# Kernel tuning notes

Hardware: AMD Instinct MI355X
Metric: run time of the kernel (lower is better)

Reference implementation:

```python
import jax, jax.numpy as jnp
import numpy as np

B, CIN, COUT, IMG = 32, 64, 64, 128


def setup_inputs() -> dict:
    key = jax.random.key(0)
    k1, k2 = jax.random.split(key, 2)
    x = jax.random.normal(k1, (B, CIN, IMG, IMG), dtype=jnp.float32)
    kernel = jax.random.uniform(k2, (COUT, 3, 3), dtype=jnp.float32)
    bias = jnp.zeros((COUT, 1, 1, 1), dtype=jnp.float32)
    return {"x": x, "kernel": kernel, "bias": bias}


def reference(x, kernel, bias):
    # GCLayer math: weight[c, ci, p, q] = kernel[c, di+1, dj+1] for q = neighbor(p)
    # within the 3x3 band (adjacency mask), zero elsewhere; shared across ci.
    # out[b,c,p] = sum_ci sum_q weight[c,ci,p,q] x[b,ci,q] + in_channels*bias[c]
    # == 3x3 cross-correlation (zero pad) of (sum over in-channels of x).
    cin = x.shape[1]
    xs = x.sum(axis=1, keepdims=True)              # [B,1,H,W]
    k = kernel[:, None, :, :]                      # [Cout,1,3,3]
    out = jax.lax.conv_general_dilated(
        xs, k, window_strides=(1, 1), padding=((1, 1), (1, 1)),
        dimension_numbers=("NCHW", "OIHW", "NCHW"))  # [B,Cout,H,W]
    # bias (out,1,1,1) was added before the in-channel sum -> scaled by cin
    out = out + cin * bias.reshape(1, -1, 1, 1)
    return out
```

## Files before the change

### kernel.cpp

```cpp
#include <hip/hip_runtime.h>

#define B_    32
#define CIN_  64
#define COUT_ 64
#define IMG_  128
#define W4_   32
#define PIX4_ 4096
#define NPOS_ (B_ * PIX4_)

__global__ __launch_bounds__(256) void ch_sum2(const float* __restrict__ x,
                                               float* __restrict__ part) {
    const int g   = blockIdx.y;
    const int tid = threadIdx.x;
    const int i0  = blockIdx.x * 512 + tid;
    const int i1  = i0 + 256;
    const int b   = i0 >> 12;
    const int p0  = i0 & (PIX4_ - 1);

    const float4* xp = reinterpret_cast<const float4*>(x)
                     + ((size_t)b * CIN_ + (size_t)g * 32) * PIX4_ + p0;

    float4 a0 = make_float4(0.f, 0.f, 0.f, 0.f);
    float4 a1 = make_float4(0.f, 0.f, 0.f, 0.f);
#pragma unroll 8
    for (int c = 0; c < 32; ++c) {
        float4 v0 = xp[(size_t)c * PIX4_];
        float4 v1 = xp[(size_t)c * PIX4_ + 256];
        a0.x += v0.x; a0.y += v0.y; a0.z += v0.z; a0.w += v0.w;
        a1.x += v1.x; a1.y += v1.y; a1.z += v1.z; a1.w += v1.w;
    }
    float4* pp = reinterpret_cast<float4*>(part) + (size_t)g * NPOS_;
    pp[i0] = a0;
    pp[i1] = a1;
}

__global__ __launch_bounds__(256) void conv_shfl(const float* __restrict__ part,
                                                 const float* __restrict__ kern,
                                                 const float* __restrict__ bias,
                                                 float* __restrict__ out) {
    const int n   = blockIdx.x;
    const int swz = (n & 7) * 512 + (n >> 3);
    const int co   = swz & 63;
    const int half = (swz >> 6) & 1;
    const int b    = swz >> 7;
    const int tid  = threadIdx.x;
    const int w4   = tid & 31;
    const int rb   = (tid >> 5) * 8;
    const int r0   = half * 64;

    const float4* p0 = reinterpret_cast<const float4*>(part) + (size_t)b * PIX4_;
    const float4* p1 = p0 + (size_t)NPOS_;

    float4 C[10];
#pragma unroll
    for (int r = 0; r < 10; ++r) {
        const int row = r0 + rb - 1 + r;
        float4 v = make_float4(0.f, 0.f, 0.f, 0.f);
        if (row >= 0 && row < IMG_) {
            float4 u0 = p0[row * W4_ + w4];
            float4 u1 = p1[row * W4_ + w4];
            v = make_float4(u0.x + u1.x, u0.y + u1.y, u0.z + u1.z, u0.w + u1.w);
        }
        C[r] = v;
    }

    float Lw[10], Rx[10];
#pragma unroll
    for (int r = 0; r < 10; ++r) {
        float lw = __shfl_up(C[r].w, 1, 32);
        float rx = __shfl_down(C[r].x, 1, 32);
        Lw[r] = (w4 > 0)  ? lw : 0.f;
        Rx[r] = (w4 < 31) ? rx : 0.f;
    }

    const float* kw = kern + co * 9;
    const float k0 = kw[0], k1 = kw[1], k2 = kw[2];
    const float k3 = kw[3], k4 = kw[4], k5 = kw[5];
    const float k6 = kw[6], k7 = kw[7], k8 = kw[8];
    const float bv = (float)CIN_ * bias[co];

    float4* outp = reinterpret_cast<float4*>(out) + (size_t)(b * COUT_ + co) * PIX4_;

#pragma unroll
    for (int j = 0; j < 8; ++j) {
        float4 a;
        a.x = bv + k0 * Lw[j]     + k1 * C[j].x     + k2 * C[j].y
                 + k3 * Lw[j + 1] + k4 * C[j + 1].x + k5 * C[j + 1].y
                 + k6 * Lw[j + 2] + k7 * C[j + 2].x + k8 * C[j + 2].y;
        a.y = bv + k0 * C[j].x     + k1 * C[j].y     + k2 * C[j].z
                 + k3 * C[j + 1].x + k4 * C[j + 1].y + k5 * C[j + 1].z
                 + k6 * C[j + 2].x + k7 * C[j + 2].y + k8 * C[j + 2].z;
        a.z = bv + k0 * C[j].y     + k1 * C[j].z     + k2 * C[j].w
                 + k3 * C[j + 1].y + k4 * C[j + 1].z + k5 * C[j + 1].w
                 + k6 * C[j + 2].y + k7 * C[j + 2].z + k8 * C[j + 2].w;
        a.w = bv + k0 * C[j].z     + k1 * C[j].w     + k2 * Rx[j]
                 + k3 * C[j + 1].z + k4 * C[j + 1].w + k5 * Rx[j + 1]
                 + k6 * C[j + 2].z + k7 * C[j + 2].w + k8 * Rx[j + 2];
        outp[(size_t)(r0 + rb + j) * W4_ + w4] = a;
    }
}

extern "C" void kernel_launch(void* const* d_in, const int* in_sizes, int n_in,
                              void* d_out, int out_size, void* d_ws, size_t ws_size,
                              hipStream_t stream) {
    const float* x    = (const float*)d_in[0];
    const float* kern = (const float*)d_in[1];
    const float* bias = (const float*)d_in[2];
    float* out  = (float*)d_out;
    float* part = (float*)d_ws;

    dim3 ga(NPOS_ / 512, 2);
    ch_sum2<<<ga, 256, 0, stream>>>(x, part);

    conv_shfl<<<dim3(B_ * COUT_ * 2), 256, 0, stream>>>(part, kern, bias, out);
}
```

Measured before the change: 60.27 us.

## Merge channel-sum and conv into one staged kernel that overlaps batch halves

Fuses the channel-reduction and conv kernels into a single kernel that picks its role from the block index, and splits the batch into two halves across three launches. The middle launch runs the channel sum for batches 16-31 alongside the conv for batches 0-15, so the read-bound reduction and the write-bound conv can overlap instead of running back to back. This adds a third launch and relies on stream ordering between launches for correctness, so each launch does less work in exchange.

```diff
diff --git a/kernel.cpp b/kernel.cpp
--- a/kernel.cpp
+++ b/kernel.cpp
@@ -8,48 +8,45 @@
 #define PIX4_ 4096
 #define NPOS_ (B_ * PIX4_)
 
-__global__ __launch_bounds__(256) void ch_sum2(const float* __restrict__ x,
-                                               float* __restrict__ part) {
-    const int g   = blockIdx.y;
-    const int tid = threadIdx.x;
-    const int i0  = blockIdx.x * 512 + tid;
-    const int i1  = i0 + 256;
-    const int b   = i0 >> 12;
-    const int p0  = i0 & (PIX4_ - 1);
+__global__ __launch_bounds__(256) void gc_stage(
+    const float* __restrict__ x, const float* __restrict__ kern,
+    const float* __restrict__ bias, float* __restrict__ out,
+    float* __restrict__ part, int na, int ab, int bb)
+{
+    const int n = blockIdx.x, tid = threadIdx.x;
 
-    const float4* xp = reinterpret_cast<const float4*>(x)
-                     + ((size_t)b * CIN_ + (size_t)g * 32) * PIX4_ + p0;
+    if (n < na) {
+        const int b = ab + (n >> 4), sub = n & 15, g = sub >> 3, q = sub & 7;
+        const int p0 = q * 512 + tid, p1 = p0 + 256;
+        const float4* xp = reinterpret_cast<const float4*>(x)
+                         + ((size_t)b * CIN_ + (size_t)g * 32) * PIX4_;
+        float4 a0 = make_float4(0.f, 0.f, 0.f, 0.f);
+        float4 a1 = make_float4(0.f, 0.f, 0.f, 0.f);
+#pragma unroll 8
+        for (int c = 0; c < 32; ++c) {
+            float4 v0 = xp[(size_t)c * PIX4_ + p0];
+            float4 v1 = xp[(size_t)c * PIX4_ + p1];
+            a0.x += v0.x; a0.y += v0.y; a0.z += v0.z; a0.w += v0.w;
+            a1.x += v1.x; a1.y += v1.y; a1.z += v1.z; a1.w += v1.w;
+        }
+        float4* pp = reinterpret_cast<float4*>(part)
+                   + (size_t)g * NPOS_ + (size_t)b * PIX4_;
+        pp[p0] = a0;
+        pp[p1] = a1;
+        return;
+    }
 
-    float4 a0 = make_float4(0.f, 0.f, 0.f, 0.f);
-    float4 a1 = make_float4(0.f, 0.f, 0.f, 0.f);
-#pragma unroll 8
-    for (int c = 0; c < 32; ++c) {
-        float4 v0 = xp[(size_t)c * PIX4_];
-        float4 v1 = xp[(size_t)c * PIX4_ + 256];
-        a0.x += v0.x; a0.y += v0.y; a0.z += v0.z; a0.w += v0.w;
-        a1.x += v1.x; a1.y += v1.y; a1.z += v1.z; a1.w += v1.w;
-    }
-    float4* pp = reinterpret_cast<float4*>(part) + (size_t)g * NPOS_;
-    pp[i0] = a0;
-    pp[i1] = a1;
-}
-
-__global__ __launch_bounds__(256) void conv_shfl(const float* __restrict__ part,
-                                                 const float* __restrict__ kern,
-                                                 const float* __restrict__ bias,
-                                                 float* __restrict__ out) {
-    const int n   = blockIdx.x;
-    const int swz = (n & 7) * 512 + (n >> 3);
+    const int m   = n - na;
+    const int swz = (m & 7) * 256 + (m >> 3);
     const int co   = swz & 63;
     const int half = (swz >> 6) & 1;
-    const int b    = swz >> 7;
-    const int tid  = threadIdx.x;
+    const int b    = bb + (swz >> 7);
     const int w4   = tid & 31;
     const int rb   = (tid >> 5) * 8;
     const int r0   = half * 64;
 
-    const float4* p0 = reinterpret_cast<const float4*>(part) + (size_t)b * PIX4_;
-    const float4* p1 = p0 + (size_t)NPOS_;
+    const float4* p0p = reinterpret_cast<const float4*>(part) + (size_t)b * PIX4_;
+    const float4* p1p = p0p + (size_t)NPOS_;
 
     float4 C[10];
 #pragma unroll
@@ -57,8 +54,8 @@
         const int row = r0 + rb - 1 + r;
         float4 v = make_float4(0.f, 0.f, 0.f, 0.f);
         if (row >= 0 && row < IMG_) {
-            float4 u0 = p0[row * W4_ + w4];
-            float4 u1 = p1[row * W4_ + w4];
+            float4 u0 = p0p[row * W4_ + w4];
+            float4 u1 = p1p[row * W4_ + w4];
             v = make_float4(u0.x + u1.x, u0.y + u1.y, u0.z + u1.z, u0.w + u1.w);
         }
         C[r] = v;
@@ -109,8 +106,10 @@
     float* out  = (float*)d_out;
     float* part = (float*)d_ws;
 
-    dim3 ga(NPOS_ / 512, 2);
-    ch_sum2<<<ga, 256, 0, stream>>>(x, part);
-
-    conv_shfl<<<dim3(B_ * COUT_ * 2), 256, 0, stream>>>(part, kern, bias, out);
+    gc_stage<<<dim3(256), 256, 0, stream>>>(x, kern, bias, out, part,
+                                            256, 0, 0);
+    gc_stage<<<dim3(256 + 2048), 256, 0, stream>>>(x, kern, bias, out, part,
+                                                   256, 16, 0);
+    gc_stage<<<dim3(2048), 256, 0, stream>>>(x, kern, bias, out, part,
+                                             0, 0, 16);
 }
```

Result: slower. 66.98 us (+11.1%).
